# Performance work log

Hardware: AMD Instinct MI355X
Metric: run time of the kernel (lower is better)

## Reference

```python
import jax, jax.numpy as jnp
import numpy as np
import math

N_NODES = 20000
N_EDGES = 640000
N_BASIS = 10
NUM_NEIGHBORS = 32.0


def _fctp_scalar_attr(x0, x1, attr, W0, W1):
    """FullyConnectedTensorProduct(irreps_in, '0e' attr) == per-irrep linear
    scaled by the scalar attribute, with e3nn fan-in normalization.
    x0: [N, mul0] scalars, x1: [N, mul1, 3] vectors, attr: [N, 1]."""
    a = attr[:, :1]
    y0 = (x0 * a) @ W0 / jnp.sqrt(jnp.asarray(W0.shape[0], x0.dtype))
    y1 = jnp.einsum('nui,uv->nvi', x1 * a[:, :, None], W1) / jnp.sqrt(jnp.asarray(W1.shape[0], x1.dtype))
    return y0, y1


def setup_inputs() -> dict:
    key = jax.random.key(0)
    ks = jax.random.split(key, 13)
    node_input = jax.random.normal(ks[0], (N_NODES, 80), jnp.float32)
    node_attr = jnp.ones((N_NODES, 1), jnp.float32)
    edge_attr = jax.random.normal(ks[1], (N_EDGES, 4), jnp.float32)
    edge_scalars = jax.random.uniform(ks[2], (N_EDGES, N_BASIS), jnp.float32)
    edge_index = jax.random.randint(ks[3], (2, N_EDGES), 0, N_NODES)
    # learned params
    W_sc0 = jax.random.normal(ks[4], (32, 32), jnp.float32)
    W_sc1 = jax.random.normal(ks[5], (16, 16), jnp.float32)
    W_l1_0 = jax.random.normal(ks[6], (32, 32), jnp.float32)
    W_l1_1 = jax.random.normal(ks[7], (16, 16), jnp.float32)
    W_fc0 = jax.random.normal(ks[8], (N_BASIS, 64), jnp.float32)
    W_fc1 = jax.random.normal(ks[9], (64, 96), jnp.float32)  # 96 = tp.weight_numel
    W_l2_0 = jax.random.normal(ks[10], (48, 32), jnp.float32)
    W_l2_1 = jax.random.normal(ks[11], (48, 16), jnp.float32)
    return dict(node_input=node_input, node_attr=node_attr, edge_attr=edge_attr,
                edge_scalars=edge_scalars, W_sc0=W_sc0, W_sc1=W_sc1,
                W_l1_0=W_l1_0, W_l1_1=W_l1_1, W_fc0=W_fc0, W_fc1=W_fc1,
                W_l2_0=W_l2_0, W_l2_1=W_l2_1, edge_index=edge_index)


def reference(node_input, node_attr, edge_attr, edge_scalars,
              W_sc0, W_sc1, W_l1_0, W_l1_1, W_fc0, W_fc1, W_l2_0, W_l2_1,
              edge_index):
    N = node_input.shape[0]
    x0 = node_input[:, :32]                     # 32x0e
    x1 = node_input[:, 32:].reshape(N, 16, 3)   # 16x1o

    # self-connection and pre-TP linear
    s0, s1 = _fctp_scalar_attr(x0, x1, node_attr, W_sc0, W_sc1)
    y0, y1 = _fctp_scalar_attr(x0, x1, node_attr, W_l1_0, W_l1_1)

    # radial MLP -> per-edge TP weights (e3nn FullyConnectedNet: no bias, fan-in norm, silu)
    h = jax.nn.silu(edge_scalars @ W_fc0 / jnp.sqrt(jnp.asarray(N_BASIS, jnp.float32)))
    w = h @ W_fc1 / jnp.sqrt(jnp.asarray(64.0, jnp.float32))  # [E, 96]
    w_a, w_b, w_c, w_d = w[:, :32], w[:, 32:64], w[:, 64:80], w[:, 80:96]

    src, dst = edge_index[0], edge_index[1]
    xs0 = y0[src]                               # [E, 32]
    xs1 = y1[src]                               # [E, 16, 3]
    e0 = edge_attr[:, :1]                       # [E, 1] 0e sh
    e1 = edge_attr[:, 1:4]                      # [E, 3] 1o sh

    # 'uvu' tensor product paths -> irreps_mid = 32x0e + 16x0e + 32x1o + 16x1o
    m_a = w_a * xs0 * e0                                    # 0e x 0e -> 0e  [E,32]
    m_b = (w_b * xs0)[:, :, None] * e1[:, None, :]          # 0e x 1o -> 1o  [E,32,3]
    m_c = w_c[:, :, None] * xs1 * e0[:, :, None]            # 1o x 0e -> 1o  [E,16,3]
    m_d = w_d * jnp.einsum('eui,ei->eu', xs1, e1) / jnp.sqrt(jnp.asarray(3.0, jnp.float32))  # 1o x 1o -> 0e [E,16]
    mid0 = jnp.concatenate([m_a, m_d], axis=1)              # [E, 48] scalars
    mid1 = jnp.concatenate([m_b, m_c], axis=1)              # [E, 48, 3] vectors

    # scatter-add into destination nodes, normalized by sqrt(num_neighbors)
    inv = 1.0 / jnp.sqrt(jnp.asarray(NUM_NEIGHBORS, jnp.float32))
    agg0 = jax.ops.segment_sum(mid0, dst, num_segments=N) * inv
    agg1 = jax.ops.segment_sum(mid1, dst, num_segments=N) * inv

    # lin2: FCTP(irreps_mid, '0e') -> irreps_out, attr == 1
    z0 = agg0 @ W_l2_0 / jnp.sqrt(jnp.asarray(48.0, jnp.float32))
    z1 = jnp.einsum('nui,uv->nvi', agg1, W_l2_1) / jnp.sqrt(jnp.asarray(48.0, jnp.float32))

    # skip mix: output_mask of sc is all ones here (all out irreps reachable)
    c_s = math.sin(math.pi / 8)
    c_x = math.cos(math.pi / 8)
    out0 = c_s * s0 + c_x * z0
    out1 = c_s * s1 + c_x * z1
    return jnp.concatenate([out0, out1.reshape(N, 48)], axis=1)
```

## Files before the change

### kernel.cpp

```cpp
#include <hip/hip_runtime.h>

#define N_NODES 20000
#define N_EDGES 640000
#define N_MT (N_EDGES/16)

typedef short short8 __attribute__((ext_vector_type(8)));
typedef float f32x4 __attribute__((ext_vector_type(4)));

__device__ __forceinline__ unsigned short f2bf(float x){
  unsigned int u = __builtin_bit_cast(unsigned int, x);
  u += 0x7fffu + ((u >> 16) & 1u);
  return (unsigned short)(u >> 16);
}

__device__ __forceinline__ void wave_lds_fence(){
  __asm__ volatile("s_waitcnt lgkmcnt(0)" ::: "memory");
}

#define HIST_BLOCKS ((N_EDGES+255)/256)
#define YN_BLOCKS   (N_NODES/16)
#define AGGZ_BLOCKS 938

__global__ void k_pre(const int* __restrict__ ei, int* __restrict__ counts,
                      const float* __restrict__ ni, const float* __restrict__ na,
                      const float* __restrict__ Wl10, const float* __restrict__ Wl11,
                      float* __restrict__ y, float4* __restrict__ aggz){
  if (blockIdx.x < HIST_BLOCKS){
    int e = blockIdx.x*256 + threadIdx.x;
    if (e < N_EDGES) atomicAdd(&counts[ei[N_EDGES + e]], 1);
    return;
  }
  if (blockIdx.x >= HIST_BLOCKS + YN_BLOCKS){
    int i = (blockIdx.x - HIST_BLOCKS - YN_BLOCKS)*256 + threadIdx.x;
    if (i < 240000){
      float4 z = {0.f,0.f,0.f,0.f};
      float4* p = aggz + (size_t)i*4;
      p[0]=z; p[1]=z; p[2]=z; p[3]=z;
    }
    return;
  }
  __shared__ float sW0[1024];
  __shared__ float sW1[256];
  __shared__ float sni[16*84];
  __shared__ float sna[16];
  const int t = threadIdx.x;
  const int nb = (blockIdx.x - HIST_BLOCKS)*16;
  for (int i=t; i<1024; i+=256) sW0[i] = Wl10[i];
  if (t < 256) sW1[t] = Wl11[t];
  for (int i=t; i<320; i+=256){
    int n = i/20, q = i - n*20;
    *(float4*)&sni[n*84 + q*4] = *(const float4*)(ni + (size_t)(nb+n)*80 + q*4);
  }
  if (t < 16) sna[t] = na[nb + t];
  __syncthreads();
  for (int i=t; i<1280; i+=256){
    int n = i/80, k = i - n*80;
    const float* row = sni + n*84;
    float a = sna[n];
    float acc = 0.f;
    if (k < 32){
      #pragma unroll
      for (int u=0; u<32; ++u) acc += row[u]*sW0[u*32+k];
      y[(size_t)nb*80 + i] = acc * a * 0.17677669529663687f;
    } else {
      int kk = k-32, v = kk/3, ii = kk - v*3;
      #pragma unroll
      for (int u=0; u<16; ++u) acc += row[32+u*3+ii]*sW1[u*16+v];
      y[(size_t)nb*80 + i] = acc * a * 0.25f;
    }
  }
}

__global__ void k_alloc(const int* __restrict__ counts, int* __restrict__ ctr,
                        int* __restrict__ cursor){
  int n = blockIdx.x*256 + threadIdx.x;
  if (n < N_NODES) cursor[n] = atomicAdd(ctr, counts[n]);
}

__global__ void k_fill(const int* __restrict__ ei, const float* __restrict__ ea,
                       const float* __restrict__ es, int* __restrict__ cursor,
                       float4* __restrict__ meta){
  int e = blockIdx.x*256 + threadIdx.x;
  if (e >= N_EDGES) return;
  int s = ei[e], d = ei[N_EDGES + e];
  int pos = atomicAdd(&cursor[d], 1);
  const float* eap = ea + (size_t)e*4;
  const float* esp = es + (size_t)e*10;
  float4 v0, v1, v2, v3;
  v0.x = eap[0]; v0.y = eap[1]; v0.z = eap[2]; v0.w = eap[3];
  v1.x = esp[0]; v1.y = esp[1]; v1.z = esp[2]; v1.w = esp[3];
  v2.x = esp[4]; v2.y = esp[5]; v2.z = esp[6]; v2.w = esp[7];
  v3.x = esp[8]; v3.y = esp[9];
  v3.z = __int_as_float(s); v3.w = __int_as_float(d);
  float4* mp = meta + (size_t)pos*4;
  mp[0] = v0; mp[1] = v1; mp[2] = v2; mp[3] = v3;
}

__global__ __launch_bounds__(256, 3) void k_edge(
    const float4* __restrict__ meta,
    const float* __restrict__ Wfc0, const float* __restrict__ Wfc1,
    const float* __restrict__ y, float* __restrict__ agg){
  __shared__ float s_wfc0[640];
  __shared__ float s_w [4][16*98];
  __shared__ float s_y [4][16*84];
  __shared__ float s_m [4][16*20];

  const int t = threadIdx.x;
  const int w = t >> 6, l = t & 63;
  const int r = l & 15, part = l >> 4;

  for (int i = t; i < 640; i += 256) s_wfc0[i] = Wfc0[i];

  short8 b0[6], b1[6];
  #pragma unroll
  for (int nt=0; nt<6; ++nt){
    #pragma unroll
    for (int j=0; j<8; ++j){
      b0[nt][j] = (short)f2bf(Wfc1[(     part*8+j)*96 + nt*16 + r]);
      b1[nt][j] = (short)f2bf(Wfc1[(32 + part*8+j)*96 + nt*16 + r]);
    }
  }
  __syncthreads();

  int o_c[3], yo[3], eai[3];
  #pragma unroll
  for (int p=0; p<3; ++p){
    int c = p*64 + l;
    if (c < 32)      { o_c[p]=c;    yo[p]=c;        eai[p]=0; }
    else if (c < 48) { int u=c-32;  o_c[p]=80+u;    yo[p]=32+3*u; eai[p]=0; }
    else if (c < 144){ int idx=c-48;  int u=idx/3, fi=idx-u*3; o_c[p]=32+u; yo[p]=u;        eai[p]=1+fi; }
    else             { int idx=c-144; int u=idx/3, i =idx-u*3; o_c[p]=64+u; yo[p]=32+3*u+i; eai[p]=0; }
  }
  const bool dot0 = (l >= 32) && (l < 48);

  float* sw = s_w[w];
  float* sy = s_y[w];
  float* sm = s_m[w];

  const int gw = blockIdx.x*4 + w;
  const int nw = gridDim.x*4;
  const int m0 = (int)(((long long)gw     * N_MT) / nw);
  const int m1 = (int)(((long long)(gw+1) * N_MT) / nw);
  if (m0 >= m1) return;

  float4 mreg = meta[(size_t)m0*64 + l];

  float acc0 = 0.f, acc1 = 0.f, acc2 = 0.f;
  int dcur = -1;

  for (int m = m0; m < m1; ++m){
    const int mnx = (m+1 < m1) ? (m+1) : m;
    float4 mnext = meta[(size_t)mnx*64 + l];

    const int isrc = __float_as_int(__shfl(mreg.z, 4*r + 3));
    const int idst = __float_as_int(__shfl(mreg.w, 4*r + 3));

    float4 yv0, yv1, yv2, yv3, yv4;
    {
      const float4* yp = (const float4*)(y + (size_t)isrc*80 + part*20);
      yv0 = yp[0]; yv1 = yp[1]; yv2 = yp[2]; yv3 = yp[3]; yv4 = yp[4];
    }
    *(float4*)(sm + (l>>2)*20 + (l&3)*4) = mreg;
    {
      float* syp = sy + r*84 + part*20;
      *(float4*)(syp     ) = yv0;
      *(float4*)(syp +  4) = yv1;
      *(float4*)(syp +  8) = yv2;
      *(float4*)(syp + 12) = yv3;
      *(float4*)(syp + 16) = yv4;
    }
    wave_lds_fence();

    const float* esr = sm + r*20 + 4;
    float hv0[8], hv1[8];
    #pragma unroll
    for (int j=0; j<8; ++j){ hv0[j]=0.f; hv1[j]=0.f; }
    #pragma unroll
    for (int k=0; k<10; ++k){
      float ev = esr[k];
      const float* wr = s_wfc0 + k*64 + part*8;
      #pragma unroll
      for (int j=0; j<8; ++j){ hv0[j] += ev*wr[j]; hv1[j] += ev*wr[32+j]; }
    }
    short8 a0, a1;
    #pragma unroll
    for (int j=0; j<8; ++j){
      float x0 = hv0[j]*0.31622776601683794f;
      float x1 = hv1[j]*0.31622776601683794f;
      a0[j] = (short)f2bf(x0/(1.f+__expf(-x0)));
      a1[j] = (short)f2bf(x1/(1.f+__expf(-x1)));
    }

    #pragma unroll
    for (int nt=0; nt<6; ++nt){
      f32x4 acc = {0.f,0.f,0.f,0.f};
      acc = __builtin_amdgcn_mfma_f32_16x16x32_bf16(a0, b0[nt], acc, 0,0,0);
      acc = __builtin_amdgcn_mfma_f32_16x16x32_bf16(a1, b1[nt], acc, 0,0,0);
      #pragma unroll
      for (int rr=0; rr<4; ++rr)
        sw[(part*4+rr)*98 + nt*16 + r] = acc[rr]*0.125f;
    }
    wave_lds_fence();

    for (int e=0; e<16; ++e){
      int de = __shfl(idst, e);
      if (de != dcur){
        if (dcur >= 0){
          unsafeAtomicAdd(&agg[(size_t)dcur*192 +       l], acc0);
          unsafeAtomicAdd(&agg[(size_t)dcur*192 +  64 + l], acc1);
          unsafeAtomicAdd(&agg[(size_t)dcur*192 + 128 + l], acc2);
        }
        acc0 = acc1 = acc2 = 0.f;
        dcur = de;
      }
      const float* sme = sm + e*20;
      const float* swe = sw + e*98;
      const float* sye = sy + e*84;
      float m0v;
      if (dot0){
        m0v = swe[o_c[0]] * (sye[yo[0]]*sme[1] + sye[yo[0]+1]*sme[2] + sye[yo[0]+2]*sme[3])
              * 0.5773502691896258f;
      } else {
        m0v = swe[o_c[0]] * sye[yo[0]] * sme[eai[0]];
      }
      acc0 += m0v;
      acc1 += swe[o_c[1]] * sye[yo[1]] * sme[eai[1]];
      acc2 += swe[o_c[2]] * sye[yo[2]] * sme[eai[2]];
    }
    wave_lds_fence();

    mreg = mnext;
  }
  if (dcur >= 0){
    unsafeAtomicAdd(&agg[(size_t)dcur*192 +       l], acc0);
    unsafeAtomicAdd(&agg[(size_t)dcur*192 +  64 + l], acc1);
    unsafeAtomicAdd(&agg[(size_t)dcur*192 + 128 + l], acc2);
  }
}

__global__ void k_finish(const float* __restrict__ ni, const float* __restrict__ na,
    const float* __restrict__ Wsc0, const float* __restrict__ Wsc1,
    const float* __restrict__ Wl20, const float* __restrict__ Wl21,
    const float* __restrict__ agg, float* __restrict__ out){
  __shared__ float sWsc0[1024];
  __shared__ float sWsc1[256];
  __shared__ float sWl20[1536];
  __shared__ float sWl21[768];
  __shared__ float sni[16*84];
  __shared__ float sag[16*196];
  __shared__ float sna[16];
  const int t = threadIdx.x;
  const int nb = blockIdx.x*16;
  for (int i=t; i<1024; i+=256) sWsc0[i] = Wsc0[i];
  if (t < 256) sWsc1[t] = Wsc1[t];
  for (int i=t; i<1536; i+=256) sWl20[i] = Wl20[i];
  for (int i=t; i<768;  i+=256) sWl21[i] = Wl21[i];
  for (int i=t; i<320;  i+=256){
    int n = i/20, q = i - n*20;
    *(float4*)&sni[n*84 + q*4] = *(const float4*)(ni + (size_t)(nb+n)*80 + q*4);
  }
  for (int i=t; i<768;  i+=256){
    int n = i/48, q = i - n*48;
    *(float4*)&sag[n*196 + q*4] = *(const float4*)(agg + (size_t)(nb+n)*192 + q*4);
  }
  if (t < 16) sna[t] = na[nb + t];
  __syncthreads();

  const float c_s = 0.3826834323650898f;
  const float c_x = 0.9238795325112867f;
  const float zscale = 0.17677669529663687f * 0.14433756729740643f;
  for (int i=t; i<1280; i+=256){
    int n = i/80, k = i - n*80;
    const float* row = sni + n*84;
    const float* ag  = sag + n*196;
    float a = sna[n];
    float s = 0.f, z = 0.f;
    if (k < 32){
      #pragma unroll
      for (int u=0; u<32; ++u) s += row[u]*sWsc0[u*32+k];
      s *= a * 0.17677669529663687f;
      #pragma unroll
      for (int u=0; u<48; ++u) z += ag[u]*sWl20[u*32+k];
    } else {
      int kk=k-32, v=kk/3, ii=kk-v*3;
      #pragma unroll
      for (int u=0; u<16; ++u) s += row[32+u*3+ii]*sWsc1[u*16+v];
      s *= a * 0.25f;
      #pragma unroll
      for (int u=0; u<48; ++u) z += ag[48+u*3+ii]*sWl21[u*16+v];
    }
    out[(size_t)nb*80 + i] = c_s*s + c_x*z*zscale;
  }
}

extern "C" void kernel_launch(void* const* d_in, const int* in_sizes, int n_in,
                              void* d_out, int out_size, void* d_ws, size_t ws_size,
                              hipStream_t stream){
  const float* node_input   = (const float*)d_in[0];
  const float* node_attr    = (const float*)d_in[1];
  const float* edge_attr    = (const float*)d_in[2];
  const float* edge_scalars = (const float*)d_in[3];
  const float* W_sc0 = (const float*)d_in[4];
  const float* W_sc1 = (const float*)d_in[5];
  const float* W_l1_0 = (const float*)d_in[6];
  const float* W_l1_1 = (const float*)d_in[7];
  const float* W_fc0 = (const float*)d_in[8];
  const float* W_fc1 = (const float*)d_in[9];
  const float* W_l2_0 = (const float*)d_in[10];
  const float* W_l2_1 = (const float*)d_in[11];
  const int* edge_index = (const int*)d_in[12];
  float* out = (float*)d_out;

  char* ws = (char*)d_ws;
  float*  y      = (float*)ws;
  float*  agg    = (float*)(ws + 6400000);
  int*    counts = (int*)(ws + 21760000);
  int*    ctr    = (int*)(ws + 21840000);
  int*    cursor = (int*)(ws + 21840064);
  float4* meta   = (float4*)(ws + 22400000);

  hipMemsetAsync(counts, 0, 80064, stream);

  k_pre  <<<HIST_BLOCKS + YN_BLOCKS + AGGZ_BLOCKS, 256, 0, stream>>>(
            edge_index, counts, node_input, node_attr, W_l1_0, W_l1_1,
            y, (float4*)agg);
  k_alloc<<<(N_NODES+255)/256, 256, 0, stream>>>(counts, ctr, cursor);
  k_fill <<<(N_EDGES+255)/256, 256, 0, stream>>>(edge_index, edge_attr, edge_scalars,
                                                 cursor, meta);
  k_edge <<<768, 256, 0, stream>>>(meta, W_fc0, W_fc1, y, agg);
  k_finish<<<YN_BLOCKS, 256, 0, stream>>>(node_input, node_attr, W_sc0, W_sc1,
                                          W_l2_0, W_l2_1, agg, out);
}
```

Before: 364.0 us.

## Store node features and edge weights in bf16 to cut gather traffic and LDS

Stores the pre-TP node features y as bf16 in global memory, which halves the per-edge gather bytes. The per-wave LDS buffers for the edge weights and the gathered features also become bf16, so the kernel uses less LDS per block. That lets it raise launch bounds to 5 blocks per CU and grow the grid from 768 to 1280 blocks. The cost is lower precision for the gathered features and the per-edge weights, plus extra conversions in the inner accumulation loop.

```diff
diff --git a/kernel.cpp b/kernel.cpp
--- a/kernel.cpp
+++ b/kernel.cpp
@@ -12,6 +12,10 @@
   u += 0x7fffu + ((u >> 16) & 1u);
   return (unsigned short)(u >> 16);
 }
+__device__ __forceinline__ float bf2f(unsigned short u){
+  unsigned int v = ((unsigned int)u) << 16;
+  return __builtin_bit_cast(float, v);
+}
 
 __device__ __forceinline__ void wave_lds_fence(){
   __asm__ volatile("s_waitcnt lgkmcnt(0)" ::: "memory");
@@ -24,7 +28,7 @@
 __global__ void k_pre(const int* __restrict__ ei, int* __restrict__ counts,
                       const float* __restrict__ ni, const float* __restrict__ na,
                       const float* __restrict__ Wl10, const float* __restrict__ Wl11,
-                      float* __restrict__ y, float4* __restrict__ aggz){
+                      unsigned short* __restrict__ y, float4* __restrict__ aggz){
   if (blockIdx.x < HIST_BLOCKS){
     int e = blockIdx.x*256 + threadIdx.x;
     if (e < N_EDGES) atomicAdd(&counts[ei[N_EDGES + e]], 1);
@@ -61,12 +65,12 @@
     if (k < 32){
       #pragma unroll
       for (int u=0; u<32; ++u) acc += row[u]*sW0[u*32+k];
-      y[(size_t)nb*80 + i] = acc * a * 0.17677669529663687f;
+      y[(size_t)nb*80 + i] = f2bf(acc * a * 0.17677669529663687f);
     } else {
       int kk = k-32, v = kk/3, ii = kk - v*3;
       #pragma unroll
       for (int u=0; u<16; ++u) acc += row[32+u*3+ii]*sW1[u*16+v];
-      y[(size_t)nb*80 + i] = acc * a * 0.25f;
+      y[(size_t)nb*80 + i] = f2bf(acc * a * 0.25f);
     }
   }
 }
@@ -96,14 +100,14 @@
   mp[0] = v0; mp[1] = v1; mp[2] = v2; mp[3] = v3;
 }
 
-__global__ __launch_bounds__(256, 3) void k_edge(
+__global__ __launch_bounds__(256, 5) void k_edge(
     const float4* __restrict__ meta,
     const float* __restrict__ Wfc0, const float* __restrict__ Wfc1,
-    const float* __restrict__ y, float* __restrict__ agg){
+    const unsigned short* __restrict__ yb, float* __restrict__ agg){
   __shared__ float s_wfc0[640];
-  __shared__ float s_w [4][16*98];
-  __shared__ float s_y [4][16*84];
-  __shared__ float s_m [4][16*20];
+  __shared__ unsigned short s_w[4][16*98];
+  __shared__ unsigned short s_y[4][16*88];
+  __shared__ float s_m[4][16*20];
 
   const int t = threadIdx.x;
   const int w = t >> 6, l = t & 63;
@@ -133,9 +137,12 @@
   }
   const bool dot0 = (l >= 32) && (l < 48);
 
-  float* sw = s_w[w];
-  float* sy = s_y[w];
+  unsigned short* sw = s_w[w];
+  unsigned short* sy = s_y[w];
   float* sm = s_m[w];
+
+  const int o0 = (part==0) ? 0 : (part==1) ? 24 : (part==2) ? 40 : 64;
+  const bool has3 = (part & 1) == 0;
 
   const int gw = blockIdx.x*4 + w;
   const int nw = gridDim.x*4;
@@ -155,20 +162,18 @@
     const int isrc = __float_as_int(__shfl(mreg.z, 4*r + 3));
     const int idst = __float_as_int(__shfl(mreg.w, 4*r + 3));
 
-    float4 yv0, yv1, yv2, yv3, yv4;
     {
-      const float4* yp = (const float4*)(y + (size_t)isrc*80 + part*20);
-      yv0 = yp[0]; yv1 = yp[1]; yv2 = yp[2]; yv3 = yp[3]; yv4 = yp[4];
+      const unsigned short* yrow = yb + (size_t)isrc*80;
+      uint4 va = *(const uint4*)(yrow + o0);
+      uint4 vb = *(const uint4*)(yrow + o0 + 8);
+      uint4 vc;
+      if (has3) vc = *(const uint4*)(yrow + o0 + 16);
+      unsigned short* syr = sy + r*88;
+      *(uint4*)(syr + o0)      = va;
+      *(uint4*)(syr + o0 + 8)  = vb;
+      if (has3) *(uint4*)(syr + o0 + 16) = vc;
     }
     *(float4*)(sm + (l>>2)*20 + (l&3)*4) = mreg;
-    {
-      float* syp = sy + r*84 + part*20;
-      *(float4*)(syp     ) = yv0;
-      *(float4*)(syp +  4) = yv1;
-      *(float4*)(syp +  8) = yv2;
-      *(float4*)(syp + 12) = yv3;
-      *(float4*)(syp + 16) = yv4;
-    }
     wave_lds_fence();
 
     const float* esr = sm + r*20 + 4;
@@ -198,7 +203,7 @@
       acc = __builtin_amdgcn_mfma_f32_16x16x32_bf16(a1, b1[nt], acc, 0,0,0);
       #pragma unroll
       for (int rr=0; rr<4; ++rr)
-        sw[(part*4+rr)*98 + nt*16 + r] = acc[rr]*0.125f;
+        sw[(part*4+rr)*98 + nt*16 + r] = f2bf(acc[rr]*0.125f);
     }
     wave_lds_fence();
 
@@ -214,18 +219,19 @@
         dcur = de;
       }
       const float* sme = sm + e*20;
-      const float* swe = sw + e*98;
-      const float* sye = sy + e*84;
+      const unsigned short* swe = sw + e*98;
+      const unsigned short* sye = sy + e*88;
       float m0v;
       if (dot0){
-        m0v = swe[o_c[0]] * (sye[yo[0]]*sme[1] + sye[yo[0]+1]*sme[2] + sye[yo[0]+2]*sme[3])
+        m0v = bf2f(swe[o_c[0]]) *
+              (bf2f(sye[yo[0]])*sme[1] + bf2f(sye[yo[0]+1])*sme[2] + bf2f(sye[yo[0]+2])*sme[3])
               * 0.5773502691896258f;
       } else {
-        m0v = swe[o_c[0]] * sye[yo[0]] * sme[eai[0]];
+        m0v = bf2f(swe[o_c[0]]) * bf2f(sye[yo[0]]) * sme[eai[0]];
       }
       acc0 += m0v;
-      acc1 += swe[o_c[1]] * sye[yo[1]] * sme[eai[1]];
-      acc2 += swe[o_c[2]] * sye[yo[2]] * sme[eai[2]];
+      acc1 += bf2f(swe[o_c[1]]) * bf2f(sye[yo[1]]) * sme[eai[1]];
+      acc2 += bf2f(swe[o_c[2]]) * bf2f(sye[yo[2]]) * sme[eai[2]];
     }
     wave_lds_fence();
 
@@ -312,12 +318,12 @@
   float* out = (float*)d_out;
 
   char* ws = (char*)d_ws;
-  float*  y      = (float*)ws;
-  float*  agg    = (float*)(ws + 6400000);
-  int*    counts = (int*)(ws + 21760000);
-  int*    ctr    = (int*)(ws + 21840000);
-  int*    cursor = (int*)(ws + 21840064);
-  float4* meta   = (float4*)(ws + 22400000);
+  unsigned short* y = (unsigned short*)ws;
+  float*  agg    = (float*)(ws + 3200000);
+  int*    counts = (int*)(ws + 18560000);
+  int*    ctr    = (int*)(ws + 18640000);
+  int*    cursor = (int*)(ws + 18640064);
+  float4* meta   = (float4*)(ws + 18720064 + 1984);
 
   hipMemsetAsync(counts, 0, 80064, stream);
 
@@ -327,7 +333,7 @@
   k_alloc<<<(N_NODES+255)/256, 256, 0, stream>>>(counts, ctr, cursor);
   k_fill <<<(N_EDGES+255)/256, 256, 0, stream>>>(edge_index, edge_attr, edge_scalars,
                                                  cursor, meta);
-  k_edge <<<768, 256, 0, stream>>>(meta, W_fc0, W_fc1, y, agg);
+  k_edge <<<1280, 256, 0, stream>>>(meta, W_fc0, W_fc1, y, agg);
   k_finish<<<YN_BLOCKS, 256, 0, stream>>>(node_input, node_attr, W_sc0, W_sc1,
                                           W_l2_0, W_l2_1, agg, out);
 }
```

Result: faster. 354.5 us (-2.6%).
